# Optimization experiments

Measured on AMD Instinct MI355X. Metric: run time of the kernel, lower is better.

Reference implementation:

```python
import jax, jax.numpy as jnp
import numpy as np

HEAD_SIZE = 64

def setup_inputs() -> dict:
    key = jax.random.key(0)
    ks = jax.random.split(key, 6)
    B, T, C = 4, 4096, 1024
    H = HEAD_SIZE
    return {
        "q": jax.random.normal(ks[0], (B, T, C), dtype=jnp.float32),
        "k": jax.random.normal(ks[1], (B, T, C), dtype=jnp.float32),
        "v": jax.random.normal(ks[2], (B, T, C), dtype=jnp.float32),
        "Wq": jax.random.normal(ks[3], (H, C), dtype=jnp.float32) * (C ** -0.5),
        "Wk": jax.random.normal(ks[4], (H, C), dtype=jnp.float32) * (C ** -0.5),
        "Wv": jax.random.normal(ks[5], (H, C), dtype=jnp.float32) * (C ** -0.5),
    }

def reference(q, k, v, Wq, Wk, Wv):
    # dropout p=0.0 -> identity (module applies F.dropout before each projection)
    T = q.shape[1]
    scale = HEAD_SIZE ** -0.5
    Q = jnp.einsum('btc,hc->bth', q, Wq)   # [B,T,H]
    K = jnp.einsum('btc,hc->bth', k, Wk)   # [B,T,H]
    V = jnp.einsum('btc,hc->bth', v, Wv)   # [B,T,H]
    scores = jnp.einsum('bth,bsh->bts', Q, K) * scale  # [B,T,T]
    # non-standard mask: tril with diagonal=1 (each query sees positions <= i+1)
    mask = jnp.tril(jnp.ones((T, T), dtype=bool), k=1)
    scores = jnp.where(mask, scores, -jnp.inf)
    # double scaling as in the original: softmax(scores * head_size**-0.5)
    weights = jax.nn.softmax(scores * scale, axis=-1)
    return jnp.einsum('bts,bsh->bth', weights, V)
```

## Files before the change

kernel.cpp:

```cpp
#include <hip/hip_runtime.h>
#include <hip/hip_bf16.h>

#define BB 4
#define TT 4096
#define CC 1024
#define HH 64

typedef _Float16 f16;
typedef __attribute__((ext_vector_type(8))) _Float16 f16x8;
typedef __attribute__((ext_vector_type(4))) _Float16 f16x4;
typedef __attribute__((ext_vector_type(4))) float f32x4;

#define MFMA32(a,b,c) __builtin_amdgcn_mfma_f32_16x16x32_f16((a),(b),(c),0,0,0)
#define MFMA16(a,b,c) __builtin_amdgcn_mfma_f32_16x16x16f16((a),(b),(c),0,0,0)

#define WF_ELEMS (3 * 32 * 4 * 64 * 8)
#define CHUNK_F16 1024
#define PB_F16 (256 * CHUNK_F16)

__global__ __launch_bounds__(64) void wrepack_kernel(
    const float* __restrict__ Wqg, const float* __restrict__ Wkg,
    const float* __restrict__ Wvg, f16* __restrict__ Wf)
{
  const int bx = blockIdx.x;
  const int nt = bx & 3;
  const int kc = (bx >> 2) & 31;
  const int p  = bx >> 7;
  const float* W = (p == 0) ? Wqg : (p == 1) ? Wkg : Wvg;
  const float sc = (p == 0) ? (1.4426950408889634f / 64.0f) : 1.0f;

  const int lane = threadIdx.x;
  const int l16 = lane & 15, quad = lane >> 4;
  const float* src = W + (size_t)(nt * 16 + l16) * CC + kc * 32 + quad * 8;
  f32x4 a = *(const f32x4*)src;
  f32x4 b = *(const f32x4*)(src + 4);
  f16x8 r;
  #pragma unroll
  for (int j = 0; j < 4; ++j) { r[j] = (f16)(a[j] * sc); r[j + 4] = (f16)(b[j] * sc); }
  *(f16x8*)(Wf + (size_t)bx * 512 + lane * 8) = r;
}

__global__ __launch_bounds__(256) void proj_kernel(
    const float* __restrict__ qg, const float* __restrict__ kg, const float* __restrict__ vg,
    const f16* __restrict__ Wf,
    f16* __restrict__ Qf, f16* __restrict__ Kf, f16* __restrict__ Vf)
{
  __shared__ f16 As[4][2][16][66];

  const float* X; f16* O; int p = blockIdx.y;
  if (p == 0)      { X = qg; O = Qf; }
  else if (p == 1) { X = kg; O = Kf; }
  else             { X = vg; O = Vf; }

  const int tid  = threadIdx.x;
  const int w    = tid >> 6;
  const int lane = tid & 63;
  const int quad = lane >> 4;
  const int l16  = lane & 15;
  const int r0   = blockIdx.x * 64 + w * 16;

  const float* Xp = X + (size_t)(r0 + (lane >> 4)) * CC + (lane & 15) * 4;
  const f16* Wbase = Wf + (size_t)p * 32 * 4 * 512 + lane * 8;

  f32x4 acc[4];
  #pragma unroll
  for (int nt = 0; nt < 4; ++nt) acc[nt] = (f32x4){0.f, 0.f, 0.f, 0.f};

  f32x4 cur[4], nxt[4];
  #pragma unroll
  for (int j = 0; j < 4; ++j) cur[j] = *(const f32x4*)(Xp + (size_t)(j * 4) * CC);

  #pragma unroll 1
  for (int it = 0; it < 16; ++it) {
    const int buf = it & 1;
    #pragma unroll
    for (int j = 0; j < 4; ++j) {
      f16x4 h;
      #pragma unroll
      for (int t = 0; t < 4; ++t) h[t] = (f16)cur[j][t];
      *(f16x4*)&As[w][buf][j * 4 + (lane >> 4)][(lane & 15) * 4] = h;
    }
    if (it < 15) {
      const int c0 = (it + 1) * 64;
      #pragma unroll
      for (int j = 0; j < 4; ++j)
        nxt[j] = *(const f32x4*)(Xp + (size_t)(j * 4) * CC + c0);
    }
    f16x8 wf[2][4];
    #pragma unroll
    for (int kk = 0; kk < 2; ++kk)
      #pragma unroll
      for (int nt = 0; nt < 4; ++nt)
        wf[kk][nt] = *(const f16x8*)(Wbase + (size_t)((it * 2 + kk) * 4 + nt) * 512);
    #pragma unroll
    for (int kk = 0; kk < 2; ++kk) {
      f16x8 af = *(const f16x8*)&As[w][buf][l16][kk * 32 + quad * 8];
      #pragma unroll
      for (int nt = 0; nt < 4; ++nt)
        acc[nt] = MFMA32(af, wf[kk][nt], acc[nt]);
    }
    #pragma unroll
    for (int j = 0; j < 4; ++j) cur[j] = nxt[j];
  }

  f16 (*Ls)[66] = As[w][0];
  #pragma unroll
  for (int nt = 0; nt < 4; ++nt)
    #pragma unroll
    for (int r = 0; r < 4; ++r)
      Ls[quad * 4 + r][nt * 16 + l16] = (f16)acc[nt][r];
  const size_t chunk = (size_t)blockIdx.x * 4 + w;
  if (p < 2) {
    #pragma unroll
    for (int h = 0; h < 2; ++h) {
      f16x8 t = *(const f16x8*)&Ls[l16][h * 32 + quad * 8];
      *(f16x8*)(O + (chunk * 2 + h) * 512 + lane * 8) = t;
    }
  } else {
    #pragma unroll
    for (int np = 0; np < 2; ++np) {
      f16x8 t;
      #pragma unroll
      for (int j = 0; j < 8; ++j)
        t[j] = Ls[quad * 4 + (j & 3)][(2 * np + (j >> 2)) * 16 + l16];
      *(f16x8*)(O + (chunk * 2 + np) * 512 + lane * 8) = t;
    }
  }
}

__device__ __forceinline__ void attn_tile(
    int b, int j, int a, int e, int wave, int quad, int l16, int lane, int sp,
    const f16* __restrict__ Qf, const f16* __restrict__ Kf, const f16* __restrict__ Vf,
    float* __restrict__ Opart, float* __restrict__ lpart)
{
  const int m0 = j * 64 + wave * 16;
  const int e_w = min(e, j + 1 + (wave == 3 ? 1 : 0));

  const f16* Qfb = Qf + (size_t)b * PB_F16;
  const f16* Kfb = Kf + (size_t)b * PB_F16 + lane * 8;
  const f16* Vfb = Vf + (size_t)b * PB_F16 + lane * 8;

  f16x8 qa0 = *(const f16x8*)(Qfb + ((size_t)(m0 >> 4) * 2 + 0) * 512 + lane * 8);
  f16x8 qa1 = *(const f16x8*)(Qfb + ((size_t)(m0 >> 4) * 2 + 1) * 512 + lane * 8);

  f32x4 o[4];
  float lsum = 0.f;
  #pragma unroll
  for (int nt = 0; nt < 4; ++nt) o[nt] = (f32x4){0.f, 0.f, 0.f, 0.f};

  f16x8 kc[8];
  int st = a;
  if (st < e_w) {
    const f16* kp = Kfb + (size_t)st * 4 * CHUNK_F16;
    #pragma unroll
    for (int ct = 0; ct < 4; ++ct) {
      kc[2 * ct]     = *(const f16x8*)(kp + ct * CHUNK_F16);
      kc[2 * ct + 1] = *(const f16x8*)(kp + ct * CHUNK_F16 + 512);
    }
  }

  while (st < e_w) {
    const int s0 = st * 64;
    f16x8 vv[4][2];
    const f16* vp = Vfb + (size_t)st * 4 * CHUNK_F16;
    #pragma unroll
    for (int ct = 0; ct < 4; ++ct) {
      vv[ct][0] = *(const f16x8*)(vp + ct * CHUNK_F16);
      vv[ct][1] = *(const f16x8*)(vp + ct * CHUNK_F16 + 512);
    }
    const bool more = (st + 1 < e_w);
    f16x8 kn[8];
    if (more) {
      const f16* kp = Kfb + (size_t)(st + 1) * 4 * CHUNK_F16;
      #pragma unroll
      for (int ct = 0; ct < 4; ++ct) {
        kn[2 * ct]     = *(const f16x8*)(kp + ct * CHUNK_F16);
        kn[2 * ct + 1] = *(const f16x8*)(kp + ct * CHUNK_F16 + 512);
      }
    }

    f32x4 sc[4];
    #pragma unroll
    for (int ct = 0; ct < 4; ++ct) {
      f32x4 z = (f32x4){0.f, 0.f, 0.f, 0.f};
      z = MFMA32(kc[2 * ct], qa0, z);
      sc[ct] = MFMA32(kc[2 * ct + 1], qa1, z);
    }

    const bool domask = (s0 + 63) > (m0 + 1);
    f16x4 pa[4];
    #pragma unroll
    for (int ct = 0; ct < 4; ++ct) {
      #pragma unroll
      for (int r = 0; r < 4; ++r) {
        float x = sc[ct][r];
        if (domask) {
          const int key = s0 + ct * 16 + quad * 4 + r;
          if (key > m0 + l16 + 1) x = -__builtin_inff();
        }
        const float pv = __builtin_amdgcn_exp2f(x);
        lsum += pv;
        pa[ct][r] = (f16)pv;
      }
    }

    #pragma unroll
    for (int ct = 0; ct < 4; ++ct) {
      #pragma unroll
      for (int np = 0; np < 2; ++np) {
        f16x4 blo = __builtin_shufflevector(vv[ct][np], vv[ct][np], 0, 1, 2, 3);
        f16x4 bhi = __builtin_shufflevector(vv[ct][np], vv[ct][np], 4, 5, 6, 7);
        o[2 * np]     = MFMA16(pa[ct], blo, o[2 * np]);
        o[2 * np + 1] = MFMA16(pa[ct], bhi, o[2 * np + 1]);
      }
    }

    if (more) {
      #pragma unroll
      for (int i = 0; i < 8; ++i) kc[i] = kn[i];
    }
    ++st;
  }

  lsum += __shfl_xor(lsum, 16, 64);
  lsum += __shfl_xor(lsum, 32, 64);
  const size_t rbase = (size_t)(sp * BB + b) * TT;
  if (quad == 0) lpart[rbase + m0 + l16] = lsum;
  #pragma unroll
  for (int nt = 0; nt < 4; ++nt)
    #pragma unroll
    for (int r = 0; r < 4; ++r)
      Opart[(rbase + m0 + quad * 4 + r) * HH + nt * 16 + l16] = o[nt][r];
}

__global__ __launch_bounds__(256) void attn_kernel(
    const f16* __restrict__ Qf, const f16* __restrict__ Kf, const f16* __restrict__ Vf,
    float* __restrict__ Opart, float* __restrict__ lpart, int S)
{
  const int pr = blockIdx.x;
  const int sp = blockIdx.y;
  const int b  = blockIdx.z;
  const int tid  = threadIdx.x;
  const int wave = tid >> 6;
  const int lane = tid & 63;
  const int quad = lane >> 4;
  const int l16  = lane & 15;

  const int j1 = pr, j2 = 63 - pr;
  const int n1 = min(j1 + 2, 64), n2 = min(j2 + 2, 64);
  const int tot = n1 + n2;
  const int lo = tot * sp / S, hi = tot * (sp + 1) / S;
  const int a1 = min(lo, n1), e1 = min(hi, n1);
  const int a2 = max(lo - n1, 0), e2 = max(hi - n1, 0);

  attn_tile(b, j1, a1, e1, wave, quad, l16, lane, sp, Qf, Kf, Vf, Opart, lpart);
  attn_tile(b, j2, a2, e2, wave, quad, l16, lane, sp, Qf, Kf, Vf, Opart, lpart);
}

__global__ __launch_bounds__(256) void combine_kernel(
    const float* __restrict__ Opart, const float* __restrict__ lpart,
    float* __restrict__ out, int S)
{
  const int idx = blockIdx.x * 256 + threadIdx.x;
  const int row = idx >> 4;
  const int c   = (idx & 15) * 4;
  float l = 0.f;
  f32x4 s = (f32x4){0.f, 0.f, 0.f, 0.f};
  for (int p = 0; p < S; ++p) {
    l += lpart[(size_t)p * BB * TT + row];
    s += *(const f32x4*)&Opart[((size_t)p * BB * TT + row) * HH + c];
  }
  const float inv = 1.0f / l;
  *(f32x4*)&out[(size_t)row * HH + c] = s * inv;
}

extern "C" void kernel_launch(void* const* d_in, const int* in_sizes, int n_in,
                              void* d_out, int out_size, void* d_ws, size_t ws_size,
                              hipStream_t stream)
{
  const float* q  = (const float*)d_in[0];
  const float* k  = (const float*)d_in[1];
  const float* v  = (const float*)d_in[2];
  const float* Wq = (const float*)d_in[3];
  const float* Wk = (const float*)d_in[4];
  const float* Wv = (const float*)d_in[5];
  float* out = (float*)d_out;

  const size_t n = (size_t)BB * TT * HH;
  const size_t need8 = (WF_ELEMS + 3 * n) * sizeof(f16)
                     + 8 * n * sizeof(float) + 8 * (size_t)BB * TT * sizeof(float);
  const int S = (ws_size >= need8) ? 8 : 4;

  f16* Wf = (f16*)d_ws;
  f16* Qf = Wf + WF_ELEMS;
  f16* Kf = Qf + n;
  f16* Vf = Kf + n;
  float* Opart = (float*)(Vf + n);
  float* lpart = Opart + (size_t)S * n;

  wrepack_kernel<<<dim3(384), 64, 0, stream>>>(Wq, Wk, Wv, Wf);
  proj_kernel<<<dim3(256, 3), 256, 0, stream>>>(q, k, v, Wf, Qf, Kf, Vf);
  attn_kernel<<<dim3(32, S, BB), 256, 0, stream>>>(Qf, Kf, Vf, Opart, lpart, S);
  combine_kernel<<<dim3(1024), 256, 0, stream>>>(Opart, lpart, out, S);
}
```

Before: 252.9 us.

## Deepen software prefetch in projection and attention loops, add occupancy hints

The projection kernel now double-buffers the weight fragments and prefetches X tiles two iterations ahead instead of one, so global loads overlap more with the MFMA work. The attention loop now prefetches the next V tile together with the next K tile rather than loading V at the top of each iteration, which hides V load latency behind the current step's compute. Both kernels get a min-blocks-per-SM launch bound of 3 to limit register use. The deeper buffering raises register pressure, and the launch bound could force spills.

Result: faster. 245.7 us (-2.8%).

```diff
diff --git a/kernel.cpp b/kernel.cpp
--- a/kernel.cpp
+++ b/kernel.cpp
@@ -40,7 +40,7 @@
   *(f16x8*)(Wf + (size_t)bx * 512 + lane * 8) = r;
 }
 
-__global__ __launch_bounds__(256) void proj_kernel(
+__global__ __launch_bounds__(256, 3) void proj_kernel(
     const float* __restrict__ qg, const float* __restrict__ kg, const float* __restrict__ vg,
     const f16* __restrict__ Wf,
     f16* __restrict__ Qf, f16* __restrict__ Kf, f16* __restrict__ Vf)
@@ -59,16 +59,26 @@
   const int l16  = lane & 15;
   const int r0   = blockIdx.x * 64 + w * 16;
 
-  const float* Xp = X + (size_t)(r0 + (lane >> 4)) * CC + (lane & 15) * 4;
+  const float* Xp = X + (size_t)(r0 + quad) * CC + l16 * 4;
   const f16* Wbase = Wf + (size_t)p * 32 * 4 * 512 + lane * 8;
 
   f32x4 acc[4];
   #pragma unroll
   for (int nt = 0; nt < 4; ++nt) acc[nt] = (f32x4){0.f, 0.f, 0.f, 0.f};
 
-  f32x4 cur[4], nxt[4];
-  #pragma unroll
-  for (int j = 0; j < 4; ++j) cur[j] = *(const f32x4*)(Xp + (size_t)(j * 4) * CC);
+  f32x4 x0[4], x1[4], x2[4];
+  f16x8 w0[2][4], w1[2][4];
+
+  #pragma unroll
+  for (int j = 0; j < 4; ++j) {
+    x0[j] = *(const f32x4*)(Xp + (size_t)(j * 4) * CC);
+    x1[j] = *(const f32x4*)(Xp + (size_t)(j * 4) * CC + 64);
+  }
+  #pragma unroll
+  for (int kk = 0; kk < 2; ++kk)
+    #pragma unroll
+    for (int nt = 0; nt < 4; ++nt)
+      w0[kk][nt] = *(const f16x8*)(Wbase + (size_t)(kk * 4 + nt) * 512);
 
   #pragma unroll 1
   for (int it = 0; it < 16; ++it) {
@@ -77,30 +87,33 @@
     for (int j = 0; j < 4; ++j) {
       f16x4 h;
       #pragma unroll
-      for (int t = 0; t < 4; ++t) h[t] = (f16)cur[j][t];
-      *(f16x4*)&As[w][buf][j * 4 + (lane >> 4)][(lane & 15) * 4] = h;
-    }
-    if (it < 15) {
-      const int c0 = (it + 1) * 64;
-      #pragma unroll
-      for (int j = 0; j < 4; ++j)
-        nxt[j] = *(const f32x4*)(Xp + (size_t)(j * 4) * CC + c0);
-    }
-    f16x8 wf[2][4];
+      for (int t = 0; t < 4; ++t) h[t] = (f16)x0[j][t];
+      *(f16x4*)&As[w][buf][j * 4 + quad][l16 * 4] = h;
+    }
+    const int pw = (it + 1 < 16) ? it + 1 : 15;
+    const int px = (it + 2 < 16) ? it + 2 : 15;
     #pragma unroll
     for (int kk = 0; kk < 2; ++kk)
       #pragma unroll
       for (int nt = 0; nt < 4; ++nt)
-        wf[kk][nt] = *(const f16x8*)(Wbase + (size_t)((it * 2 + kk) * 4 + nt) * 512);
+        w1[kk][nt] = *(const f16x8*)(Wbase + (size_t)((pw * 2 + kk) * 4 + nt) * 512);
+    #pragma unroll
+    for (int j = 0; j < 4; ++j)
+      x2[j] = *(const f32x4*)(Xp + (size_t)(j * 4) * CC + px * 64);
     #pragma unroll
     for (int kk = 0; kk < 2; ++kk) {
       f16x8 af = *(const f16x8*)&As[w][buf][l16][kk * 32 + quad * 8];
       #pragma unroll
       for (int nt = 0; nt < 4; ++nt)
-        acc[nt] = MFMA32(af, wf[kk][nt], acc[nt]);
-    }
-    #pragma unroll
-    for (int j = 0; j < 4; ++j) cur[j] = nxt[j];
+        acc[nt] = MFMA32(af, w0[kk][nt], acc[nt]);
+    }
+    #pragma unroll
+    for (int j = 0; j < 4; ++j) { x0[j] = x1[j]; x1[j] = x2[j]; }
+    #pragma unroll
+    for (int kk = 0; kk < 2; ++kk)
+      #pragma unroll
+      for (int nt = 0; nt < 4; ++nt)
+        w0[kk][nt] = w1[kk][nt];
   }
 
   f16 (*Ls)[66] = As[w][0];
@@ -148,34 +161,33 @@
   #pragma unroll
   for (int nt = 0; nt < 4; ++nt) o[nt] = (f32x4){0.f, 0.f, 0.f, 0.f};
 
-  f16x8 kc[8];
+  f16x8 kc[8], vc[8];
   int st = a;
   if (st < e_w) {
     const f16* kp = Kfb + (size_t)st * 4 * CHUNK_F16;
+    const f16* vp = Vfb + (size_t)st * 4 * CHUNK_F16;
     #pragma unroll
     for (int ct = 0; ct < 4; ++ct) {
       kc[2 * ct]     = *(const f16x8*)(kp + ct * CHUNK_F16);
       kc[2 * ct + 1] = *(const f16x8*)(kp + ct * CHUNK_F16 + 512);
+      vc[2 * ct]     = *(const f16x8*)(vp + ct * CHUNK_F16);
+      vc[2 * ct + 1] = *(const f16x8*)(vp + ct * CHUNK_F16 + 512);
     }
   }
 
   while (st < e_w) {
     const int s0 = st * 64;
-    f16x8 vv[4][2];
-    const f16* vp = Vfb + (size_t)st * 4 * CHUNK_F16;
-    #pragma unroll
-    for (int ct = 0; ct < 4; ++ct) {
-      vv[ct][0] = *(const f16x8*)(vp + ct * CHUNK_F16);
-      vv[ct][1] = *(const f16x8*)(vp + ct * CHUNK_F16 + 512);
-    }
     const bool more = (st + 1 < e_w);
-    f16x8 kn[8];
+    f16x8 kn[8], vn[8];
     if (more) {
       const f16* kp = Kfb + (size_t)(st + 1) * 4 * CHUNK_F16;
+      const f16* vp = Vfb + (size_t)(st + 1) * 4 * CHUNK_F16;
       #pragma unroll
       for (int ct = 0; ct < 4; ++ct) {
         kn[2 * ct]     = *(const f16x8*)(kp + ct * CHUNK_F16);
         kn[2 * ct + 1] = *(const f16x8*)(kp + ct * CHUNK_F16 + 512);
+        vn[2 * ct]     = *(const f16x8*)(vp + ct * CHUNK_F16);
+        vn[2 * ct + 1] = *(const f16x8*)(vp + ct * CHUNK_F16 + 512);
       }
     }
 
@@ -208,8 +220,8 @@
     for (int ct = 0; ct < 4; ++ct) {
       #pragma unroll
       for (int np = 0; np < 2; ++np) {
-        f16x4 blo = __builtin_shufflevector(vv[ct][np], vv[ct][np], 0, 1, 2, 3);
-        f16x4 bhi = __builtin_shufflevector(vv[ct][np], vv[ct][np], 4, 5, 6, 7);
+        f16x4 blo = __builtin_shufflevector(vc[2 * ct + np], vc[2 * ct + np], 0, 1, 2, 3);
+        f16x4 bhi = __builtin_shufflevector(vc[2 * ct + np], vc[2 * ct + np], 4, 5, 6, 7);
         o[2 * np]     = MFMA16(pa[ct], blo, o[2 * np]);
         o[2 * np + 1] = MFMA16(pa[ct], bhi, o[2 * np + 1]);
       }
@@ -217,7 +229,7 @@
 
     if (more) {
       #pragma unroll
-      for (int i = 0; i < 8; ++i) kc[i] = kn[i];
+      for (int i = 0; i < 8; ++i) { kc[i] = kn[i]; vc[i] = vn[i]; }
     }
     ++st;
   }
@@ -233,7 +245,7 @@
       Opart[(rbase + m0 + quad * 4 + r) * HH + nt * 16 + l16] = o[nt][r];
 }
 
-__global__ __launch_bounds__(256) void attn_kernel(
+__global__ __launch_bounds__(256, 3) void attn_kernel(
     const f16* __restrict__ Qf, const f16* __restrict__ Kf, const f16* __restrict__ Vf,
     float* __restrict__ Opart, float* __restrict__ lpart, int S)
 {
```

## Stage projection and attention K/V tiles through LDS with async global-to-LDS loads

Applied to the files above, without the earlier changes.

The projection kernel now streams fp32 X rows and f16 weight fragments into double-buffered shared memory via global_load_lds, using an XOR swizzle, and converts to f16 at read time. The attention kernel now loads each K/V tile into shared memory once per block and shares it across the four waves, instead of each wave fetching its own copy into registers. This is meant to cut redundant global traffic and register pressure. In exchange it adds a __syncthreads per tile, and waves can no longer skip tiles past their own causal bound, so masked work rises slightly. The global_load_lds calls have no explicit wait before the barrier, so correctness relies on the compiler inserting the vmcnt waits.

Measured after the change: 235.5 us. -6.9%, faster.

```diff
diff --git a/kernel.cpp b/kernel.cpp
--- a/kernel.cpp
+++ b/kernel.cpp
@@ -17,6 +17,19 @@
 #define WF_ELEMS (3 * 32 * 4 * 64 * 8)
 #define CHUNK_F16 1024
 #define PB_F16 (256 * CHUNK_F16)
+
+static __device__ __forceinline__ void gl_lds16(const void* g, void* l) {
+  __builtin_amdgcn_global_load_lds(
+      (const __attribute__((address_space(1))) unsigned int*)g,
+      (__attribute__((address_space(3))) unsigned int*)l, 16, 0, 0);
+}
+
+static __device__ __forceinline__ f16x8 pack2(f32x4 a, f32x4 b) {
+  f16x8 r;
+  r[0]=(f16)a[0]; r[1]=(f16)a[1]; r[2]=(f16)a[2]; r[3]=(f16)a[3];
+  r[4]=(f16)b[0]; r[5]=(f16)b[1]; r[6]=(f16)b[2]; r[7]=(f16)b[3];
+  return r;
+}
 
 __global__ __launch_bounds__(64) void wrepack_kernel(
     const float* __restrict__ Wqg, const float* __restrict__ Wkg,
@@ -45,9 +58,10 @@
     const f16* __restrict__ Wf,
     f16* __restrict__ Qf, f16* __restrict__ Kf, f16* __restrict__ Vf)
 {
-  __shared__ f16 As[4][2][16][66];
-
-  const float* X; f16* O; int p = blockIdx.y;
+  __shared__ float Xs[2][64][64];
+  __shared__ f16   Ws[2][8][64][8];
+
+  const float* X; f16* O; const int p = blockIdx.y;
   if (p == 0)      { X = qg; O = Qf; }
   else if (p == 1) { X = kg; O = Kf; }
   else             { X = vg; O = Vf; }
@@ -57,53 +71,60 @@
   const int lane = tid & 63;
   const int quad = lane >> 4;
   const int l16  = lane & 15;
-  const int r0   = blockIdx.x * 64 + w * 16;
-
-  const float* Xp = X + (size_t)(r0 + (lane >> 4)) * CC + (lane & 15) * 4;
-  const f16* Wbase = Wf + (size_t)p * 32 * 4 * 512 + lane * 8;
+  const int r0   = blockIdx.x * 64;
+
+  const float* Xrow[4];
+  #pragma unroll
+  for (int s = 0; s < 4; ++s) {
+    const int R  = w * 16 + s * 4 + (lane >> 4);
+    const int lc = (lane & 15) ^ ((R & 7) << 1);
+    Xrow[s] = X + (size_t)(r0 + R) * CC + lc * 4;
+  }
+  const f16* Wfp = Wf + (size_t)p * 128 * 512;
+  const f16* Wsrc[2];
+  #pragma unroll
+  for (int jj = 0; jj < 2; ++jj)
+    Wsrc[jj] = Wfp + (size_t)(2 * w + jj) * 512 + lane * 8;
 
   f32x4 acc[4];
   #pragma unroll
   for (int nt = 0; nt < 4; ++nt) acc[nt] = (f32x4){0.f, 0.f, 0.f, 0.f};
 
-  f32x4 cur[4], nxt[4];
-  #pragma unroll
-  for (int j = 0; j < 4; ++j) cur[j] = *(const f32x4*)(Xp + (size_t)(j * 4) * CC);
-
-  #pragma unroll 1
+  #pragma unroll
+  for (int s = 0; s < 4; ++s)
+    gl_lds16(Xrow[s], &Xs[0][w * 16 + s * 4][0]);
+  #pragma unroll
+  for (int jj = 0; jj < 2; ++jj)
+    gl_lds16(Wsrc[jj], &Ws[0][2 * w + jj][0][0]);
+
+  const int sw = (l16 & 7) << 1;
+
   for (int it = 0; it < 16; ++it) {
     const int buf = it & 1;
-    #pragma unroll
-    for (int j = 0; j < 4; ++j) {
-      f16x4 h;
-      #pragma unroll
-      for (int t = 0; t < 4; ++t) h[t] = (f16)cur[j][t];
-      *(f16x4*)&As[w][buf][j * 4 + (lane >> 4)][(lane & 15) * 4] = h;
-    }
+    __syncthreads();
     if (it < 15) {
-      const int c0 = (it + 1) * 64;
-      #pragma unroll
-      for (int j = 0; j < 4; ++j)
-        nxt[j] = *(const f32x4*)(Xp + (size_t)(j * 4) * CC + c0);
-    }
-    f16x8 wf[2][4];
-    #pragma unroll
-    for (int kk = 0; kk < 2; ++kk)
-      #pragma unroll
-      for (int nt = 0; nt < 4; ++nt)
-        wf[kk][nt] = *(const f16x8*)(Wbase + (size_t)((it * 2 + kk) * 4 + nt) * 512);
+      #pragma unroll
+      for (int s = 0; s < 4; ++s)
+        gl_lds16(Xrow[s] + (it + 1) * 64, &Xs[buf ^ 1][w * 16 + s * 4][0]);
+      #pragma unroll
+      for (int jj = 0; jj < 2; ++jj)
+        gl_lds16(Wsrc[jj] + (size_t)(it + 1) * 4096, &Ws[buf ^ 1][2 * w + jj][0][0]);
+    }
     #pragma unroll
     for (int kk = 0; kk < 2; ++kk) {
-      f16x8 af = *(const f16x8*)&As[w][buf][l16][kk * 32 + quad * 8];
-      #pragma unroll
-      for (int nt = 0; nt < 4; ++nt)
-        acc[nt] = MFMA32(af, wf[kk][nt], acc[nt]);
-    }
-    #pragma unroll
-    for (int j = 0; j < 4; ++j) cur[j] = nxt[j];
-  }
-
-  f16 (*Ls)[66] = As[w][0];
+      const int c0 = kk * 8 + quad * 2;
+      f32x4 a0 = *(const f32x4*)&Xs[buf][w * 16 + l16][(c0 ^ sw) * 4];
+      f32x4 a1 = *(const f32x4*)&Xs[buf][w * 16 + l16][((c0 + 1) ^ sw) * 4];
+      f16x8 af = pack2(a0, a1);
+      #pragma unroll
+      for (int nt = 0; nt < 4; ++nt) {
+        f16x8 bf = *(const f16x8*)&Ws[buf][kk * 4 + nt][lane][0];
+        acc[nt] = MFMA32(af, bf, acc[nt]);
+      }
+    }
+  }
+
+  f16 (*Ls)[66] = (f16(*)[66])&Xs[0][w * 16][0];
   #pragma unroll
   for (int nt = 0; nt < 4; ++nt)
     #pragma unroll
@@ -131,14 +152,14 @@
 __device__ __forceinline__ void attn_tile(
     int b, int j, int a, int e, int wave, int quad, int l16, int lane, int sp,
     const f16* __restrict__ Qf, const f16* __restrict__ Kf, const f16* __restrict__ Vf,
+    f16 (*Ks)[8][64][8], f16 (*Vs)[8][64][8],
     float* __restrict__ Opart, float* __restrict__ lpart)
 {
   const int m0 = j * 64 + wave * 16;
-  const int e_w = min(e, j + 1 + (wave == 3 ? 1 : 0));
-
+
+  const f16* Kfb = Kf + (size_t)b * PB_F16;
+  const f16* Vfb = Vf + (size_t)b * PB_F16;
   const f16* Qfb = Qf + (size_t)b * PB_F16;
-  const f16* Kfb = Kf + (size_t)b * PB_F16 + lane * 8;
-  const f16* Vfb = Vf + (size_t)b * PB_F16 + lane * 8;
 
   f16x8 qa0 = *(const f16x8*)(Qfb + ((size_t)(m0 >> 4) * 2 + 0) * 512 + lane * 8);
   f16x8 qa1 = *(const f16x8*)(Qfb + ((size_t)(m0 >> 4) * 2 + 1) * 512 + lane * 8);
@@ -148,43 +169,38 @@
   #pragma unroll
   for (int nt = 0; nt < 4; ++nt) o[nt] = (f32x4){0.f, 0.f, 0.f, 0.f};
 
-  f16x8 kc[8];
-  int st = a;
-  if (st < e_w) {
-    const f16* kp = Kfb + (size_t)st * 4 * CHUNK_F16;
+  __syncthreads();
+
+  if (a < e) {
+    #pragma unroll
+    for (int jj = 0; jj < 2; ++jj) {
+      const int idx = 2 * wave + jj;
+      gl_lds16(Kfb + (size_t)a * 4096 + idx * 512 + lane * 8, &Ks[0][idx][0][0]);
+      gl_lds16(Vfb + (size_t)a * 4096 + idx * 512 + lane * 8, &Vs[0][idx][0][0]);
+    }
+  }
+
+  for (int st = a; st < e; ++st) {
+    const int buf = (st - a) & 1;
+    __syncthreads();
+    if (st + 1 < e) {
+      #pragma unroll
+      for (int jj = 0; jj < 2; ++jj) {
+        const int idx = 2 * wave + jj;
+        gl_lds16(Kfb + (size_t)(st + 1) * 4096 + idx * 512 + lane * 8, &Ks[buf ^ 1][idx][0][0]);
+        gl_lds16(Vfb + (size_t)(st + 1) * 4096 + idx * 512 + lane * 8, &Vs[buf ^ 1][idx][0][0]);
+      }
+    }
+    const int s0 = st * 64;
+
+    f32x4 sc[4];
     #pragma unroll
     for (int ct = 0; ct < 4; ++ct) {
-      kc[2 * ct]     = *(const f16x8*)(kp + ct * CHUNK_F16);
-      kc[2 * ct + 1] = *(const f16x8*)(kp + ct * CHUNK_F16 + 512);
-    }
-  }
-
-  while (st < e_w) {
-    const int s0 = st * 64;
-    f16x8 vv[4][2];
-    const f16* vp = Vfb + (size_t)st * 4 * CHUNK_F16;
-    #pragma unroll
-    for (int ct = 0; ct < 4; ++ct) {
-      vv[ct][0] = *(const f16x8*)(vp + ct * CHUNK_F16);
-      vv[ct][1] = *(const f16x8*)(vp + ct * CHUNK_F16 + 512);
-    }
-    const bool more = (st + 1 < e_w);
-    f16x8 kn[8];
-    if (more) {
-      const f16* kp = Kfb + (size_t)(st + 1) * 4 * CHUNK_F16;
-      #pragma unroll
-      for (int ct = 0; ct < 4; ++ct) {
-        kn[2 * ct]     = *(const f16x8*)(kp + ct * CHUNK_F16);
-        kn[2 * ct + 1] = *(const f16x8*)(kp + ct * CHUNK_F16 + 512);
-      }
-    }
-
-    f32x4 sc[4];
-    #pragma unroll
-    for (int ct = 0; ct < 4; ++ct) {
+      f16x8 k0 = *(const f16x8*)&Ks[buf][ct * 2][lane][0];
+      f16x8 k1 = *(const f16x8*)&Ks[buf][ct * 2 + 1][lane][0];
       f32x4 z = (f32x4){0.f, 0.f, 0.f, 0.f};
-      z = MFMA32(kc[2 * ct], qa0, z);
-      sc[ct] = MFMA32(kc[2 * ct + 1], qa1, z);
+      z = MFMA32(k0, qa0, z);
+      sc[ct] = MFMA32(k1, qa1, z);
     }
 
     const bool domask = (s0 + 63) > (m0 + 1);
@@ -208,18 +224,13 @@
     for (int ct = 0; ct < 4; ++ct) {
       #pragma unroll
       for (int np = 0; np < 2; ++np) {
-        f16x4 blo = __builtin_shufflevector(vv[ct][np], vv[ct][np], 0, 1, 2, 3);
-        f16x4 bhi = __builtin_shufflevector(vv[ct][np], vv[ct][np], 4, 5, 6, 7);
+        f16x8 vv = *(const f16x8*)&Vs[buf][ct * 2 + np][lane][0];
+        f16x4 blo = __builtin_shufflevector(vv, vv, 0, 1, 2, 3);
+        f16x4 bhi = __builtin_shufflevector(vv, vv, 4, 5, 6, 7);
         o[2 * np]     = MFMA16(pa[ct], blo, o[2 * np]);
         o[2 * np + 1] = MFMA16(pa[ct], bhi, o[2 * np + 1]);
       }
     }
-
-    if (more) {
-      #pragma unroll
-      for (int i = 0; i < 8; ++i) kc[i] = kn[i];
-    }
-    ++st;
   }
 
   lsum += __shfl_xor(lsum, 16, 64);
@@ -237,6 +248,9 @@
     const f16* __restrict__ Qf, const f16* __restrict__ Kf, const f16* __restrict__ Vf,
     float* __restrict__ Opart, float* __restrict__ lpart, int S)
 {
+  __shared__ f16 Ks[2][8][64][8];
+  __shared__ f16 Vs[2][8][64][8];
+
   const int pr = blockIdx.x;
   const int sp = blockIdx.y;
   const int b  = blockIdx.z;
@@ -253,8 +267,8 @@
   const int a1 = min(lo, n1), e1 = min(hi, n1);
   const int a2 = max(lo - n1, 0), e2 = max(hi - n1, 0);
 
-  attn_tile(b, j1, a1, e1, wave, quad, l16, lane, sp, Qf, Kf, Vf, Opart, lpart);
-  attn_tile(b, j2, a2, e2, wave, quad, l16, lane, sp, Qf, Kf, Vf, Opart, lpart);
+  attn_tile(b, j1, a1, e1, wave, quad, l16, lane, sp, Qf, Kf, Vf, Ks, Vs, Opart, lpart);
+  attn_tile(b, j2, a2, e2, wave, quad, l16, lane, sp, Qf, Kf, Vf, Ks, Vs, Opart, lpart);
 }
 
 __global__ __launch_bounds__(256) void combine_kernel(
```
